# Optimization experiments

Measured on AMD Instinct MI355X. Metric: run time of the kernel, lower is better.

## Reference

```python
import jax, jax.numpy as jnp
import numpy as np

H = 128        # hidden_size == embed dim
HEADS = 8
HD = H // HEADS  # 16
OUT = 2


def _mlp(x, w1, b1, w2, b2, w3, b3):
    # build_mlps(2, [128, 64, 128], ret_before_act=True, without_norm=True)
    x = jax.nn.relu(x @ w1.T + b1)
    x = jax.nn.relu(x @ w2.T + b2)
    return x @ w3.T + b3


def _cross_attn(q, kv, mask, wq, bq, wk, bk, wv, bv, wo, bo):
    # q: [B, A, H] agent queries; kv: [B, M, H] map polylines; mask: [B, M] True = padded
    B, A, _ = q.shape
    M = kv.shape[1]
    qh = (q @ wq.T + bq).reshape(B, A, HEADS, HD)
    kh = (kv @ wk.T + bk).reshape(B, M, HEADS, HD)
    vh = (kv @ wv.T + bv).reshape(B, M, HEADS, HD)
    scores = jnp.einsum('bahd,bmhd->bham', qh, kh) * (1.0 / np.sqrt(HD))
    scores = jnp.where(mask[:, None, None, :], jnp.finfo(scores.dtype).min, scores)
    attn = jax.nn.softmax(scores, axis=-1)
    out = jnp.einsum('bham,bmhd->bahd', attn, vh).reshape(B, A, H)
    return out @ wo.T + bo


def _lstm_cell(x, h, c, avail, w_ih, w_hh, b_ih, b_hh):
    # standard torch LSTMCell math, masked update per agent availability
    gates = x @ w_ih.T + b_ih + h @ w_hh.T + b_hh
    i, f, g, o = jnp.split(gates, 4, axis=-1)
    c_new = jax.nn.sigmoid(f) * c + jax.nn.sigmoid(i) * jnp.tanh(g)
    h_new = jax.nn.sigmoid(o) * jnp.tanh(c_new)
    m = avail[..., None]
    return jnp.where(m, h_new, h), jnp.where(m, c_new, c)


def setup_inputs() -> dict:
    key = jax.random.key(0)
    B, A, M, T = 128, 64, 512, 80
    ks = jax.random.split(key, 32)
    p = lambda k, shape: (jax.random.normal(k, shape, dtype=jnp.float32) * 0.02)
    map_avails = jax.random.uniform(ks[5], (B, M)) > 0.2
    map_avails = map_avails.at[:, :8].set(True)  # guarantee non-empty attention rows
    return {
        'current_features': jax.random.normal(ks[0], (B, A, 2), dtype=jnp.float32),
        'current_availabilities': jnp.ones((B, A), dtype=bool),
        'hidden': jax.random.normal(ks[1], (B, A, H), dtype=jnp.float32),
        'context': jax.random.normal(ks[2], (B, A, H), dtype=jnp.float32),
        'map_embedding': jax.random.normal(ks[3], (B, M, H), dtype=jnp.float32),
        'map_avails': map_avails,
        'n_timesteps': T,
        # state encoder MLP: 2 -> 128 -> 64 -> 128
        'enc_w1': p(ks[6], (128, 2)),  'enc_b1': jnp.zeros((128,), jnp.float32),
        'enc_w2': p(ks[7], (64, 128)), 'enc_b2': jnp.zeros((64,), jnp.float32),
        'enc_w3': p(ks[8], (128, 64)), 'enc_b3': jnp.zeros((128,), jnp.float32),
        # cross-attention projections
        'wq': p(ks[9], (H, H)),  'bq': jnp.zeros((H,), jnp.float32),
        'wk': p(ks[10], (H, H)), 'bk': jnp.zeros((H,), jnp.float32),
        'wv': p(ks[11], (H, H)), 'bv': jnp.zeros((H,), jnp.float32),
        'wo': p(ks[12], (H, H)), 'bo': jnp.zeros((H,), jnp.float32),
        # LSTM cell (input 128, hidden 128)
        'w_ih': p(ks[13], (4 * H, H)), 'w_hh': p(ks[14], (4 * H, H)),
        'b_ih': jnp.zeros((4 * H,), jnp.float32), 'b_hh': jnp.zeros((4 * H,), jnp.float32),
        # output head
        'lin_w': p(ks[15], (OUT, H)), 'lin_b': jnp.zeros((OUT,), jnp.float32),
    }


def reference(current_features, current_availabilities, hidden, context,
              map_embedding, map_avails, n_timesteps,
              enc_w1, enc_b1, enc_w2, enc_b2, enc_w3, enc_b3,
              wq, bq, wk, bk, wv, bv, wo, bo,
              w_ih, w_hh, b_ih, b_hh, lin_w, lin_b):
    state0 = current_features[..., :2]
    cross_mask = ~map_avails

    def step(carry, _):
        state, h, c = carry
        e = _mlp(state, enc_w1, enc_b1, enc_w2, enc_b2, enc_w3, enc_b3)
        e = _cross_attn(e, map_embedding, cross_mask, wq, bq, wk, bk, wv, bv, wo, bo)
        h, c = _lstm_cell(e, h, c, current_availabilities, w_ih, w_hh, b_ih, b_hh)
        state = state + h @ lin_w.T + lin_b
        return (state, h, c), state

    _, ys = jax.lax.scan(step, (state0, hidden, context), None, length=n_timesteps)
    return jnp.moveaxis(ys, 0, 2)  # [B, A, T, 2]
```

## Files before the change

kernel.cpp:

```cpp
#include <hip/hip_runtime.h>
#include <cstdint>
#include <cstddef>


typedef short short8 __attribute__((ext_vector_type(8)));
typedef float f32x4 __attribute__((ext_vector_type(4)));

#define LOG2E 1.4426950408889634f
#define QSCALE 0.36067376022224085f

__device__ __forceinline__ unsigned short f2bf(float f) {
  union { float f; unsigned int u; } v; v.f = f;
  unsigned int u = v.u;
  return (unsigned short)((u + 0x7fffu + ((u >> 16) & 1u)) >> 16);
}
__device__ __forceinline__ float fexp2(float x) {
  return __builtin_amdgcn_exp2f(x);
}
__device__ __forceinline__ float frcp(float x) {
  return __builtin_amdgcn_rcpf(x);
}
__device__ __forceinline__ float sigm(float x) {
  return frcp(1.f + fexp2(-LOG2E * x));
}
__device__ __forceinline__ float tanh_f(float x) {
  return 1.f - 2.f * frcp(1.f + fexp2(2.f * LOG2E * x));
}
__device__ __forceinline__ f32x4 splat4(float v) { f32x4 r = {v, v, v, v}; return r; }
__device__ __forceinline__ unsigned char f2fp8(float x) {
  return (unsigned char)__builtin_amdgcn_cvt_pk_fp8_f32(x, x, 0, false);
}
__device__ __forceinline__ f32x4 mfma_fp8(long a, long b, f32x4 c) {
  return __builtin_amdgcn_mfma_f32_16x16x32_fp8_fp8(a, b, c, 0, 0, 0);
}
__device__ __forceinline__ f32x4 mfma_bf16(short8 a, short8 b, f32x4 c) {
  return __builtin_amdgcn_mfma_f32_16x16x32_bf16(a, b, c, 0, 0, 0);
}

__global__ __launch_bounds__(256) void convert_kernel(
    const float* __restrict__ w2, const float* __restrict__ whh,
    unsigned short* __restrict__ W2, unsigned short* __restrict__ WHH) {
  int i = blockIdx.x * 256 + threadIdx.x;
  if (i >= 73728) return;
  if (i < 8192) W2[i] = f2bf(w2[i]);
  else          WHH[i - 8192] = f2bf(whh[i - 8192]);
}

__global__ __launch_bounds__(256) void fold_wiho_kernel(
    const float* __restrict__ wih, const float* __restrict__ wo,
    unsigned short* __restrict__ WIHO) {
  int i = blockIdx.x * 256 + threadIdx.x;
  int r = i >> 7, d = i & 127;
  float acc = 0.f;
  for (int n = 0; n < 128; ++n) acc = fmaf(wih[r * 128 + n], wo[n * 128 + d], acc);
  WIHO[i] = f2bf(acc);
}

__global__ __launch_bounds__(256) void fold_wq3b_kernel(
    const float* __restrict__ wq, const float* __restrict__ w3,
    const float* __restrict__ b3, const float* __restrict__ bq,
    const float* __restrict__ wih, const float* __restrict__ bo,
    const float* __restrict__ bih, const float* __restrict__ bhh,
    unsigned short* __restrict__ WQ3, float* __restrict__ B4p,
    float* __restrict__ BQ3S) {
  int i = blockIdx.x * 256 + threadIdx.x;
  if (i < 8192) {
    int n = i >> 6, k = i & 63;
    float acc = 0.f;
    for (int j = 0; j < 128; ++j) acc = fmaf(wq[n * 128 + j], w3[j * 64 + k], acc);
    WQ3[i] = f2bf(acc * QSCALE);
  } else if (i < 8704) {
    int r = i - 8192;
    float acc = bih[r] + bhh[r];
    for (int n = 0; n < 128; ++n) acc = fmaf(wih[r * 128 + n], bo[n], acc);
    B4p[r] = acc;
  } else if (i < 8832) {
    int n = i - 8704;
    float acc = bq[n];
    for (int j = 0; j < 128; ++j) acc = fmaf(wq[n * 128 + j], b3[j], acc);
    BQ3S[n] = acc * QSCALE;
  }
}

__global__ __launch_bounds__(256) void kv_kernel(
    const float* __restrict__ emb, const float* __restrict__ wk,
    const float* __restrict__ bk, const float* __restrict__ wv,
    const float* __restrict__ bv,
    unsigned char* __restrict__ K8, unsigned char* __restrict__ V8) {
  extern __shared__ char smem[];
  float* s_e = (float*)smem;
  float* s_w = (float*)(smem + 33024);
  const int tid = threadIdx.x;
  const int b = blockIdx.x >> 3;
  const int m0 = (blockIdx.x & 7) * 64;

  for (int i = tid; i < 8192; i += 256) {
    int row = i >> 7, col = i & 127;
    s_e[row * 129 + col] = emb[(size_t)(b * 512 + m0 + row) * 128 + col];
  }
  for (int i = tid; i < 16384; i += 256) {
    int row = i >> 7, col = i & 127;
    s_w[row * 129 + col] = wk[i];
  }
  __syncthreads();
  {
    const int dg = tid & 31, rg = tid >> 5;
    float acc[8][4];
#pragma unroll
    for (int rr = 0; rr < 8; ++rr)
#pragma unroll
      for (int j = 0; j < 4; ++j) acc[rr][j] = 0.f;
    for (int k = 0; k < 128; ++k) {
      float e[8];
#pragma unroll
      for (int rr = 0; rr < 8; ++rr) e[rr] = s_e[(rg * 8 + rr) * 129 + k];
#pragma unroll
      for (int j = 0; j < 4; ++j) {
        float w = s_w[(dg * 4 + j) * 129 + k];
#pragma unroll
        for (int rr = 0; rr < 8; ++rr) acc[rr][j] = fmaf(e[rr], w, acc[rr][j]);
      }
    }
#pragma unroll
    for (int rr = 0; rr < 8; ++rr)
#pragma unroll
      for (int j = 0; j < 4; ++j) {
        int d = dg * 4 + j;
        K8[(size_t)(b * 512 + m0 + rg * 8 + rr) * 128 + d] = f2fp8(acc[rr][j] + bk[d]);
      }
  }
  __syncthreads();
  for (int i = tid; i < 16384; i += 256) {
    int row = i >> 7, col = i & 127;
    s_w[row * 129 + col] = wv[i];
  }
  __syncthreads();
  {
    const int r = tid & 63, dg = tid >> 6;
    float acc[32];
#pragma unroll
    for (int j = 0; j < 32; ++j) acc[j] = 0.f;
    for (int k = 0; k < 128; ++k) {
      float e = s_e[r * 129 + k];
#pragma unroll
      for (int j = 0; j < 32; ++j) acc[j] = fmaf(e, s_w[(dg * 32 + j) * 129 + k], acc[j]);
    }
    const int m = m0 + r;
    const int ml = m & 31;
    const int sperm = (ml < 16) ? (((ml >> 2) << 3) | (ml & 3))
                                : ((((ml - 16) >> 2) << 3) | ((ml - 16) & 3) | 4);
    const int mpos = (m & ~31) | sperm;
#pragma unroll
    for (int j = 0; j < 32; ++j) {
      int d = dg * 32 + j;
      V8[(size_t)(b * 128 + d) * 512 + mpos] = f2fp8(acc[j] + bv[d]);
    }
  }
}

__global__ __launch_bounds__(512, 2) void decoder_kernel(
    const float* __restrict__ cf, const int* __restrict__ cav,
    const float* __restrict__ hid,
    const float* __restrict__ ctx, const int* __restrict__ mav,
    const int* __restrict__ ntp,
    const float* __restrict__ w1, const float* __restrict__ b1,
    const float* __restrict__ b2,
    const unsigned char* __restrict__ K8, const unsigned char* __restrict__ V8,
    const unsigned short* __restrict__ W2, const unsigned short* __restrict__ WQ3,
    const unsigned short* __restrict__ WIHO, const unsigned short* __restrict__ WHH,
    const float* __restrict__ B4p, const float* __restrict__ BQ3S,
    const float* __restrict__ lnw, const float* __restrict__ lnb,
    float* __restrict__ out) {
  extern __shared__ char smem[];
  unsigned short* s_bufA = (unsigned short*)(smem + 131072);
  unsigned short* s_bufB = (unsigned short*)(smem + 139776);
  unsigned short* s_h = (unsigned short*)(smem + 148480);
  unsigned short* s_h2 = (unsigned short*)(smem + 157184);
  unsigned char* s_maskb = (unsigned char*)(smem + 162048);

  const int tid = threadIdx.x;
  const int wave = tid >> 6;
  const int lane = tid & 63;
  const int quad = lane >> 4;
  const int l16 = lane & 15;

  const int b = blockIdx.x & 127;
  const int a0 = (blockIdx.x >> 7) * 32;
  const int T = *ntp;
  const f32x4 zero4 = {0.f, 0.f, 0.f, 0.f};
  const long kOnes = 0x3838383838383838L;

  {
    const unsigned long long* Kg = (const unsigned long long*)(K8 + (size_t)b * 65536);
    for (int i = tid; i < 8192; i += 512) {
      int tok = i >> 4, seg = i & 15;
      *(unsigned long long*)(smem + tok * 128 + ((seg * 8) ^ ((tok & 15) * 8))) =
          Kg[(size_t)tok * 16 + seg];
    }
    const unsigned long long* Vg = (const unsigned long long*)(V8 + (size_t)b * 65536);
    for (int i = tid; i < 8192; i += 512) {
      int d = i >> 6, seg = i & 63;
      *(unsigned long long*)(smem + 65536 + d * 512 + ((seg * 8) ^ ((d & 15) * 8))) =
          Vg[(size_t)d * 64 + seg];
    }
  }
  s_maskb[tid] = mav[b * 512 + tid] ? 1 : 0;
  {
    int idx = tid * 8;
    int a = idx >> 7, n0 = idx & 127;
    const float* hp = hid + (size_t)(b * 64 + a0 + a) * 128 + n0;
    short8 v;
#pragma unroll
    for (int j = 0; j < 8; ++j) v[j] = (short)f2bf(hp[j]);
    *(short8*)(s_h + a * 136 + n0) = v;
  }
  float c_reg[2][4], avl[2][4];
#pragma unroll
  for (int mt = 0; mt < 2; ++mt)
#pragma unroll
    for (int r = 0; r < 4; ++r) {
      int a = mt * 16 + quad * 4 + r;
      c_reg[mt][r] = ctx[(size_t)(b * 64 + a0 + a) * 128 + wave * 16 + l16];
      avl[mt][r] = (cav[b * 64 + a0 + a] != 0) ? 1.f : 0.f;
    }

  const int wrow = wave * 16 + l16;
  short8 rIH[4][4], rHH[4][4];
#pragma unroll
  for (int kt = 0; kt < 4; ++kt)
#pragma unroll
    for (int g = 0; g < 4; ++g) {
      rIH[kt][g] = *(const short8*)(WIHO + ((g * 128 + wrow) * 128 + kt * 32 + quad * 8));
      rHH[kt][g] = *(const short8*)(WHH + ((g * 128 + wrow) * 128 + kt * 32 + quad * 8));
    }
  short8 rWQ3[2];
#pragma unroll
  for (int kt = 0; kt < 2; ++kt)
    rWQ3[kt] = *(const short8*)(WQ3 + (wrow * 64 + kt * 32 + quad * 8));
  float rB4[4];
#pragma unroll
  for (int g = 0; g < 4; ++g) rB4[g] = B4p[g * 128 + wrow];
  const float rBQ3 = BQ3S[wrow];
  const float rB2 = b2[(wave & 3) * 16 + l16];

  const int p7_o = tid >> 3, p7_sub = tid & 7;
  const int p7_a = p7_o >> 1, p7_oi = p7_o & 1;
  const float mylnb = lnb[p7_oi];
  float myst = cf[(size_t)(b * 64 + a0 + p7_a) * 2 + p7_oi];

  __syncthreads();

  unsigned mflags = 0;
#pragma unroll
  for (int i = 0; i < 32; ++i)
    if (!s_maskb[i * 16 + l16]) mflags |= (1u << i);

  {
    float other = __shfl_xor(myst, 8);
    float st0 = p7_oi ? other : myst;
    float st1 = p7_oi ? myst : other;
    int a = tid >> 4, n0 = (tid & 15) * 8;
    const float* wp = w1 + n0 * 2;
    const float* bp = b1 + n0;
    short8 v;
#pragma unroll
    for (int j = 0; j < 8; ++j) {
      float x = fmaf(wp[j * 2], st0, fmaf(wp[j * 2 + 1], st1, bp[j]));
      v[j] = (short)f2bf(fmaxf(x, 0.f));
    }
    *(short8*)(s_bufA + a * 136 + n0) = v;
  }
  __syncthreads();

#pragma unroll 1
  for (int t = 0; t < T; ++t) {
    {
      int mt = wave >> 2, nt = wave & 3;
      f32x4 acc = splat4(rB2);
#pragma unroll
      for (int kt = 0; kt < 4; ++kt) {
        short8 a8 = *(const short8*)(s_bufA + (mt * 16 + l16) * 136 + kt * 32 + quad * 8);
        short8 b8 = *(const short8*)(W2 + ((nt * 16 + l16) * 128 + kt * 32 + quad * 8));
        acc = mfma_bf16(a8, b8, acc);
      }
#pragma unroll
      for (int r = 0; r < 4; ++r)
        s_h2[(mt * 16 + quad * 4 + r) * 72 + nt * 16 + l16] = f2bf(fmaxf(acc[r], 0.f));
    }
    __syncthreads();

    unsigned char* s_q8 = (unsigned char*)s_bufA;
    {
#pragma unroll
      for (int mt = 0; mt < 2; ++mt) {
        f32x4 acc = splat4(rBQ3);
#pragma unroll
        for (int kt = 0; kt < 2; ++kt) {
          short8 a8 = *(const short8*)(s_h2 + (mt * 16 + l16) * 72 + kt * 32 + quad * 8);
          acc = mfma_bf16(a8, rWQ3[kt], acc);
        }
#pragma unroll
        for (int r = 0; r < 4; ++r)
          s_q8[(mt * 16 + quad * 4 + r) * 136 + wave * 16 + l16] = f2fp8(acc[r]);
      }
    }
    __asm__ volatile("s_waitcnt lgkmcnt(0)" ::: "memory");
    __builtin_amdgcn_sched_barrier(0);

    {
      const int h = wave;
      const char* sKb = (const char*)smem;
      const char* sVrow = (const char*)(smem + 65536) + (h * 16 + l16) * 512;
      long qA[2];
#pragma unroll
      for (int mt = 0; mt < 2; ++mt)
        qA[mt] = (quad < 2)
                     ? *(const long*)(s_q8 + (mt * 16 + l16) * 136 + h * 16 + quad * 8)
                     : (quad == 2 ? 0xF8L : 0L);
      const int koff = (h * 16 + quad * 8) ^ (l16 * 8);
      f32x4 O[2], L4[2];
      O[0] = zero4; O[1] = zero4; L4[0] = zero4; L4[1] = zero4;
      long vA_c = *(const long*)(sVrow + ((quad * 8) ^ (l16 * 8)));
      long kB_c0 = 0L, kB_c1 = 0L;
      if (quad < 2) {
        kB_c0 = *(const long*)(sKb + (size_t)l16 * 128 + koff);
        kB_c1 = *(const long*)(sKb + (size_t)(16 + l16) * 128 + koff);
      }
#pragma unroll 4
      for (int c = 0; c < 16; ++c) {
        long vA_n = 0L, kB_n0 = 0L, kB_n1 = 0L;
        if (c < 15) {
          vA_n = *(const long*)(sVrow + (((c + 1) * 32 + quad * 8) ^ (l16 * 8)));
          if (quad < 2) {
            kB_n0 = *(const long*)(sKb + (size_t)((c + 1) * 32 + l16) * 128 + koff);
            kB_n1 = *(const long*)(sKb + (size_t)((c + 1) * 32 + 16 + l16) * 128 + koff);
          }
        }
        long kB0 = kB_c0, kB1 = kB_c1;
        if (quad == 2) {
          kB0 = ((mflags >> (c * 2)) & 1u) ? 0x38L : 0L;
          kB1 = ((mflags >> (c * 2 + 1)) & 1u) ? 0x38L : 0L;
        }
        f32x4 S2[2][2];
        S2[0][0] = mfma_fp8(kB0, qA[0], zero4);
        S2[0][1] = mfma_fp8(kB0, qA[1], zero4);
        S2[1][0] = mfma_fp8(kB1, qA[0], zero4);
        S2[1][1] = mfma_fp8(kB1, qA[1], zero4);
#pragma unroll
        for (int mt = 0; mt < 2; ++mt) {
          unsigned w0 = (unsigned)__builtin_amdgcn_cvt_pk_fp8_f32(
              fexp2(S2[0][mt][0]), fexp2(S2[0][mt][1]), 0, false);
          w0 = (unsigned)__builtin_amdgcn_cvt_pk_fp8_f32(
              fexp2(S2[0][mt][2]), fexp2(S2[0][mt][3]), (int)w0, true);
          unsigned w1v = (unsigned)__builtin_amdgcn_cvt_pk_fp8_f32(
              fexp2(S2[1][mt][0]), fexp2(S2[1][mt][1]), 0, false);
          w1v = (unsigned)__builtin_amdgcn_cvt_pk_fp8_f32(
              fexp2(S2[1][mt][2]), fexp2(S2[1][mt][3]), (int)w1v, true);
          long pB = (long)(((unsigned long long)w1v << 32) | (unsigned long long)w0);
          O[mt] = mfma_fp8(vA_c, pB, O[mt]);
          L4[mt] = mfma_fp8(kOnes, pB, L4[mt]);
        }
        vA_c = vA_n; kB_c0 = kB_n0; kB_c1 = kB_n1;
      }
#pragma unroll
      for (int mt = 0; mt < 2; ++mt) {
        unsigned long long ow = 0;
#pragma unroll
        for (int r = 0; r < 4; ++r) {
          float o_r = O[mt][r] * frcp(L4[mt][r]);
          ow |= (unsigned long long)f2bf(o_r) << (16 * r);
        }
        *(unsigned long long*)(s_bufB + (mt * 16 + l16) * 136 + h * 16 + quad * 4) = ow;
      }
    }
    __syncthreads();

    {
      const int ni = wave;
      f32x4 gi[2], gf[2], gg[2], go[2];
#pragma unroll
      for (int mt = 0; mt < 2; ++mt) {
        gi[mt] = splat4(rB4[0]);
        gf[mt] = splat4(rB4[1]);
        gg[mt] = splat4(rB4[2]);
        go[mt] = splat4(rB4[3]);
      }
#pragma unroll
      for (int kt = 0; kt < 4; ++kt)
#pragma unroll
        for (int mt = 0; mt < 2; ++mt) {
          short8 a8 = *(const short8*)(s_bufB + (mt * 16 + l16) * 136 + kt * 32 + quad * 8);
          gi[mt] = mfma_bf16(a8, rIH[kt][0], gi[mt]);
          gf[mt] = mfma_bf16(a8, rIH[kt][1], gf[mt]);
          gg[mt] = mfma_bf16(a8, rIH[kt][2], gg[mt]);
          go[mt] = mfma_bf16(a8, rIH[kt][3], go[mt]);
        }
#pragma unroll
      for (int kt = 0; kt < 4; ++kt)
#pragma unroll
        for (int mt = 0; mt < 2; ++mt) {
          short8 a8 = *(const short8*)(s_h + (mt * 16 + l16) * 136 + kt * 32 + quad * 8);
          gi[mt] = mfma_bf16(a8, rHH[kt][0], gi[mt]);
          gf[mt] = mfma_bf16(a8, rHH[kt][1], gf[mt]);
          gg[mt] = mfma_bf16(a8, rHH[kt][2], gg[mt]);
          go[mt] = mfma_bf16(a8, rHH[kt][3], go[mt]);
        }
      float hnew[2][4];
#pragma unroll
      for (int mt = 0; mt < 2; ++mt)
#pragma unroll
        for (int r = 0; r < 4; ++r) {
          float iv = sigm(gi[mt][r]);
          float fv = sigm(gf[mt][r]);
          float gv = tanh_f(gg[mt][r]);
          float ov = sigm(go[mt][r]);
          float cn = fmaf(fv, c_reg[mt][r], iv * gv);
          float hv = ov * tanh_f(cn);
          int arow = mt * 16 + quad * 4 + r;
          float av = avl[mt][r];
          union { unsigned int u; float f; } ho;
          ho.u = ((unsigned int)s_h[arow * 136 + ni * 16 + l16]) << 16;
          c_reg[mt][r] = av * cn + (1.f - av) * c_reg[mt][r];
          hnew[mt][r] = av * hv + (1.f - av) * ho.f;
        }
      __syncthreads();
#pragma unroll
      for (int mt = 0; mt < 2; ++mt)
#pragma unroll
        for (int r = 0; r < 4; ++r) {
          int arow = mt * 16 + quad * 4 + r;
          s_h[arow * 136 + ni * 16 + l16] = f2bf(hnew[mt][r]);
        }
    }
    __syncthreads();

    {
      const unsigned short* hp = s_h + p7_a * 136 + p7_sub * 16;
      const float* lw = lnw + p7_oi * 128 + p7_sub * 16;
      short8 h0 = *(const short8*)hp;
      short8 h1 = *(const short8*)(hp + 8);
      float acc = 0.f;
#pragma unroll
      for (int k = 0; k < 8; ++k) {
        union { unsigned int u; float f; } hv;
        hv.u = ((unsigned int)(unsigned short)h0[k]) << 16;
        acc = fmaf(hv.f, lw[k], acc);
      }
#pragma unroll
      for (int k = 0; k < 8; ++k) {
        union { unsigned int u; float f; } hv;
        hv.u = ((unsigned int)(unsigned short)h1[k]) << 16;
        acc = fmaf(hv.f, lw[8 + k], acc);
      }
      acc += __shfl_xor(acc, 4);
      acc += __shfl_xor(acc, 2);
      acc += __shfl_xor(acc, 1);
      float ns = myst + acc + mylnb;
      myst = ns;
      if (p7_sub == 0)
        out[((size_t)(b * 64 + a0 + p7_a) * T + t) * 2 + p7_oi] = ns;
      float other = __shfl_xor(ns, 8);
      float st0 = p7_oi ? other : ns;
      float st1 = p7_oi ? ns : other;
      int a = tid >> 4, n0 = (tid & 15) * 8;
      const float* wp = w1 + n0 * 2;
      const float* bp = b1 + n0;
      short8 v;
#pragma unroll
      for (int j = 0; j < 8; ++j) {
        float x = fmaf(wp[j * 2], st0, fmaf(wp[j * 2 + 1], st1, bp[j]));
        v[j] = (short)f2bf(fmaxf(x, 0.f));
      }
      *(short8*)(s_bufA + a * 136 + n0) = v;
    }
    __syncthreads();
  }
}

extern "C" void kernel_launch(void* const* d_in, const int* in_sizes, int n_in,
                              void* d_out, int out_size, void* d_ws, size_t ws_size,
                              hipStream_t stream) {
  (void)in_sizes; (void)n_in; (void)out_size; (void)ws_size;
  const float* cf = (const float*)d_in[0];
  const int* cav = (const int*)d_in[1];
  const float* hid = (const float*)d_in[2];
  const float* ctx = (const float*)d_in[3];
  const float* emb = (const float*)d_in[4];
  const int* mav = (const int*)d_in[5];
  const int* ntp = (const int*)d_in[6];
  const float* w1 = (const float*)d_in[7];
  const float* b1 = (const float*)d_in[8];
  const float* w2 = (const float*)d_in[9];
  const float* b2 = (const float*)d_in[10];
  const float* w3 = (const float*)d_in[11];
  const float* b3 = (const float*)d_in[12];
  const float* wq = (const float*)d_in[13];
  const float* bq = (const float*)d_in[14];
  const float* wk = (const float*)d_in[15];
  const float* bk = (const float*)d_in[16];
  const float* wv = (const float*)d_in[17];
  const float* bv = (const float*)d_in[18];
  const float* wo = (const float*)d_in[19];
  const float* bo = (const float*)d_in[20];
  const float* wih = (const float*)d_in[21];
  const float* whh = (const float*)d_in[22];
  const float* bih = (const float*)d_in[23];
  const float* bhh = (const float*)d_in[24];
  const float* lnw = (const float*)d_in[25];
  const float* lnb = (const float*)d_in[26];

  char* ws = (char*)d_ws;
  unsigned char* K8 = (unsigned char*)(ws + 0);
  unsigned char* V8 = (unsigned char*)(ws + 8388608);
  unsigned short* W2s = (unsigned short*)(ws + 16777216);
  unsigned short* WQ3s = (unsigned short*)(ws + 16793600);
  unsigned short* WIHOs = (unsigned short*)(ws + 16809984);
  unsigned short* WHHs = (unsigned short*)(ws + 16941056);
  float* B4p = (float*)(ws + 17072128);
  float* BQ3S = (float*)(ws + 17074176);

  (void)hipFuncSetAttribute((const void*)kv_kernel,
                            hipFuncAttributeMaxDynamicSharedMemorySize, 99072);
  (void)hipFuncSetAttribute((const void*)decoder_kernel,
                            hipFuncAttributeMaxDynamicSharedMemorySize, 162560);

  convert_kernel<<<288, 256, 0, stream>>>(w2, whh, W2s, WHHs);
  fold_wiho_kernel<<<256, 256, 0, stream>>>(wih, wo, WIHOs);
  fold_wq3b_kernel<<<35, 256, 0, stream>>>(wq, w3, b3, bq, wih, bo, bih, bhh,
                                           WQ3s, B4p, BQ3S);
  kv_kernel<<<1024, 256, 99072, stream>>>(emb, wk, bk, wv, bv, K8, V8);
  decoder_kernel<<<256, 512, 162560, stream>>>(
      cf, cav, hid, ctx, mav, ntp, w1, b1, b2, K8, V8, W2s, WQ3s, WIHOs, WHHs,
      B4p, BQ3S, lnw, lnb, (float*)d_out);
}
```

Baseline: 1.293 ms.

## Merge prep kernels into one launch and software-pipeline the decoder step

Combines the four preprocessing kernels into one prep_kernel launch, dispatched by block index, to cut launch overhead. In the decoder's attention loop, score MFMAs are issued one chunk ahead and K loads two chunks ahead, to hide latency. Hidden-state fragments are loaded into registers at the start of each step, which lets the LSTM write the new h directly and drops one __syncthreads. The extra live registers may hurt occupancy, and prep blocks now all reserve the large shared-memory allocation.

```diff
diff --git a/kernel.cpp b/kernel.cpp
--- a/kernel.cpp
+++ b/kernel.cpp
@@ -37,123 +37,122 @@
   return __builtin_amdgcn_mfma_f32_16x16x32_bf16(a, b, c, 0, 0, 0);
 }
 
-__global__ __launch_bounds__(256) void convert_kernel(
-    const float* __restrict__ w2, const float* __restrict__ whh,
-    unsigned short* __restrict__ W2, unsigned short* __restrict__ WHH) {
-  int i = blockIdx.x * 256 + threadIdx.x;
-  if (i >= 73728) return;
-  if (i < 8192) W2[i] = f2bf(w2[i]);
-  else          WHH[i - 8192] = f2bf(whh[i - 8192]);
-}
-
-__global__ __launch_bounds__(256) void fold_wiho_kernel(
-    const float* __restrict__ wih, const float* __restrict__ wo,
-    unsigned short* __restrict__ WIHO) {
-  int i = blockIdx.x * 256 + threadIdx.x;
-  int r = i >> 7, d = i & 127;
-  float acc = 0.f;
-  for (int n = 0; n < 128; ++n) acc = fmaf(wih[r * 128 + n], wo[n * 128 + d], acc);
-  WIHO[i] = f2bf(acc);
-}
-
-__global__ __launch_bounds__(256) void fold_wq3b_kernel(
-    const float* __restrict__ wq, const float* __restrict__ w3,
-    const float* __restrict__ b3, const float* __restrict__ bq,
-    const float* __restrict__ wih, const float* __restrict__ bo,
-    const float* __restrict__ bih, const float* __restrict__ bhh,
-    unsigned short* __restrict__ WQ3, float* __restrict__ B4p,
-    float* __restrict__ BQ3S) {
-  int i = blockIdx.x * 256 + threadIdx.x;
-  if (i < 8192) {
-    int n = i >> 6, k = i & 63;
-    float acc = 0.f;
-    for (int j = 0; j < 128; ++j) acc = fmaf(wq[n * 128 + j], w3[j * 64 + k], acc);
-    WQ3[i] = f2bf(acc * QSCALE);
-  } else if (i < 8704) {
-    int r = i - 8192;
-    float acc = bih[r] + bhh[r];
-    for (int n = 0; n < 128; ++n) acc = fmaf(wih[r * 128 + n], bo[n], acc);
-    B4p[r] = acc;
-  } else if (i < 8832) {
-    int n = i - 8704;
-    float acc = bq[n];
-    for (int j = 0; j < 128; ++j) acc = fmaf(wq[n * 128 + j], b3[j], acc);
-    BQ3S[n] = acc * QSCALE;
-  }
-}
-
-__global__ __launch_bounds__(256) void kv_kernel(
+__global__ __launch_bounds__(256) void prep_kernel(
     const float* __restrict__ emb, const float* __restrict__ wk,
     const float* __restrict__ bk, const float* __restrict__ wv,
     const float* __restrict__ bv,
-    unsigned char* __restrict__ K8, unsigned char* __restrict__ V8) {
+    const float* __restrict__ w2, const float* __restrict__ whh,
+    const float* __restrict__ wih, const float* __restrict__ wo,
+    const float* __restrict__ wq, const float* __restrict__ w3,
+    const float* __restrict__ b3, const float* __restrict__ bq,
+    const float* __restrict__ bo, const float* __restrict__ bih,
+    const float* __restrict__ bhh,
+    unsigned char* __restrict__ K8, unsigned char* __restrict__ V8,
+    unsigned short* __restrict__ W2, unsigned short* __restrict__ WHH,
+    unsigned short* __restrict__ WIHO, unsigned short* __restrict__ WQ3,
+    float* __restrict__ B4p, float* __restrict__ BQ3S) {
   extern __shared__ char smem[];
-  float* s_e = (float*)smem;
-  float* s_w = (float*)(smem + 33024);
   const int tid = threadIdx.x;
-  const int b = blockIdx.x >> 3;
-  const int m0 = (blockIdx.x & 7) * 64;
-
-  for (int i = tid; i < 8192; i += 256) {
-    int row = i >> 7, col = i & 127;
-    s_e[row * 129 + col] = emb[(size_t)(b * 512 + m0 + row) * 128 + col];
-  }
-  for (int i = tid; i < 16384; i += 256) {
-    int row = i >> 7, col = i & 127;
-    s_w[row * 129 + col] = wk[i];
-  }
-  __syncthreads();
-  {
-    const int dg = tid & 31, rg = tid >> 5;
-    float acc[8][4];
-#pragma unroll
-    for (int rr = 0; rr < 8; ++rr)
-#pragma unroll
-      for (int j = 0; j < 4; ++j) acc[rr][j] = 0.f;
-    for (int k = 0; k < 128; ++k) {
-      float e[8];
-#pragma unroll
-      for (int rr = 0; rr < 8; ++rr) e[rr] = s_e[(rg * 8 + rr) * 129 + k];
-#pragma unroll
-      for (int j = 0; j < 4; ++j) {
-        float w = s_w[(dg * 4 + j) * 129 + k];
-#pragma unroll
-        for (int rr = 0; rr < 8; ++rr) acc[rr][j] = fmaf(e[rr], w, acc[rr][j]);
-      }
-    }
-#pragma unroll
-    for (int rr = 0; rr < 8; ++rr)
-#pragma unroll
-      for (int j = 0; j < 4; ++j) {
-        int d = dg * 4 + j;
-        K8[(size_t)(b * 512 + m0 + rg * 8 + rr) * 128 + d] = f2fp8(acc[rr][j] + bk[d]);
-      }
-  }
-  __syncthreads();
-  for (int i = tid; i < 16384; i += 256) {
-    int row = i >> 7, col = i & 127;
-    s_w[row * 129 + col] = wv[i];
-  }
-  __syncthreads();
-  {
-    const int r = tid & 63, dg = tid >> 6;
-    float acc[32];
-#pragma unroll
-    for (int j = 0; j < 32; ++j) acc[j] = 0.f;
-    for (int k = 0; k < 128; ++k) {
-      float e = s_e[r * 129 + k];
-#pragma unroll
-      for (int j = 0; j < 32; ++j) acc[j] = fmaf(e, s_w[(dg * 32 + j) * 129 + k], acc[j]);
-    }
-    const int m = m0 + r;
-    const int ml = m & 31;
-    const int sperm = (ml < 16) ? (((ml >> 2) << 3) | (ml & 3))
-                                : ((((ml - 16) >> 2) << 3) | ((ml - 16) & 3) | 4);
-    const int mpos = (m & ~31) | sperm;
-#pragma unroll
-    for (int j = 0; j < 32; ++j) {
-      int d = dg * 32 + j;
-      V8[(size_t)(b * 128 + d) * 512 + mpos] = f2fp8(acc[j] + bv[d]);
+  const int blk = blockIdx.x;
+
+  if (blk < 1024) {
+    float* s_e = (float*)smem;
+    float* s_w = (float*)(smem + 33024);
+    const int b = blk >> 3;
+    const int m0 = (blk & 7) * 64;
+
+    for (int i = tid; i < 8192; i += 256) {
+      int row = i >> 7, col = i & 127;
+      s_e[row * 129 + col] = emb[(size_t)(b * 512 + m0 + row) * 128 + col];
+    }
+    for (int i = tid; i < 16384; i += 256) {
+      int row = i >> 7, col = i & 127;
+      s_w[row * 129 + col] = wk[i];
+    }
+    __syncthreads();
+    {
+      const int dg = tid & 31, rg = tid >> 5;
+      float acc[8][4];
+#pragma unroll
+      for (int rr = 0; rr < 8; ++rr)
+#pragma unroll
+        for (int j = 0; j < 4; ++j) acc[rr][j] = 0.f;
+      for (int k = 0; k < 128; ++k) {
+        float e[8];
+#pragma unroll
+        for (int rr = 0; rr < 8; ++rr) e[rr] = s_e[(rg * 8 + rr) * 129 + k];
+#pragma unroll
+        for (int j = 0; j < 4; ++j) {
+          float w = s_w[(dg * 4 + j) * 129 + k];
+#pragma unroll
+          for (int rr = 0; rr < 8; ++rr) acc[rr][j] = fmaf(e[rr], w, acc[rr][j]);
+        }
+      }
+#pragma unroll
+      for (int rr = 0; rr < 8; ++rr)
+#pragma unroll
+        for (int j = 0; j < 4; ++j) {
+          int d = dg * 4 + j;
+          K8[(size_t)(b * 512 + m0 + rg * 8 + rr) * 128 + d] =
+              f2fp8(acc[rr][j] + bk[d]);
+        }
+    }
+    __syncthreads();
+    for (int i = tid; i < 16384; i += 256) {
+      int row = i >> 7, col = i & 127;
+      s_w[row * 129 + col] = wv[i];
+    }
+    __syncthreads();
+    {
+      const int r = tid & 63, dg = tid >> 6;
+      float acc[32];
+#pragma unroll
+      for (int j = 0; j < 32; ++j) acc[j] = 0.f;
+      for (int k = 0; k < 128; ++k) {
+        float e = s_e[r * 129 + k];
+#pragma unroll
+        for (int j = 0; j < 32; ++j)
+          acc[j] = fmaf(e, s_w[(dg * 32 + j) * 129 + k], acc[j]);
+      }
+      const int m = m0 + r;
+      const int ml = m & 31;
+      const int sperm = (ml < 16) ? (((ml >> 2) << 3) | (ml & 3))
+                                  : ((((ml - 16) >> 2) << 3) | ((ml - 16) & 3) | 4);
+      const int mpos = (m & ~31) | sperm;
+#pragma unroll
+      for (int j = 0; j < 32; ++j) {
+        int d = dg * 32 + j;
+        V8[(size_t)(b * 128 + d) * 512 + mpos] = f2fp8(acc[j] + bv[d]);
+      }
+    }
+  } else if (blk < 1280) {
+    int i = (blk - 1024) * 256 + tid;
+    int r = i >> 7, d = i & 127;
+    float acc = 0.f;
+    for (int n = 0; n < 128; ++n)
+      acc = fmaf(wih[r * 128 + n], wo[n * 128 + d], acc);
+    WIHO[i] = f2bf(acc);
+  } else if (blk < 1568) {
+    int i = (blk - 1280) * 256 + tid;
+    if (i < 8192) W2[i] = f2bf(w2[i]);
+    else if (i < 73728) WHH[i - 8192] = f2bf(whh[i - 8192]);
+  } else {
+    int i = (blk - 1568) * 256 + tid;
+    if (i < 8192) {
+      int n = i >> 6, k = i & 63;
+      float acc = 0.f;
+      for (int j = 0; j < 128; ++j) acc = fmaf(wq[n * 128 + j], w3[j * 64 + k], acc);
+      WQ3[i] = f2bf(acc * QSCALE);
+    } else if (i < 8704) {
+      int r = i - 8192;
+      float acc = bih[r] + bhh[r];
+      for (int n = 0; n < 128; ++n) acc = fmaf(wih[r * 128 + n], bo[n], acc);
+      B4p[r] = acc;
+    } else if (i < 8832) {
+      int n = i - 8704;
+      float acc = bq[n];
+      for (int j = 0; j < 128; ++j) acc = fmaf(wq[n * 128 + j], b3[j], acc);
+      BQ3S[n] = acc * QSCALE;
     }
   }
 }
@@ -274,6 +273,22 @@
 
 #pragma unroll 1
   for (int t = 0; t < T; ++t) {
+    short8 rHa[4][2];
+    float hoF[2][4];
+#pragma unroll
+    for (int kt = 0; kt < 4; ++kt)
+#pragma unroll
+      for (int mt = 0; mt < 2; ++mt)
+        rHa[kt][mt] = *(const short8*)(s_h + (mt * 16 + l16) * 136 + kt * 32 + quad * 8);
+#pragma unroll
+    for (int mt = 0; mt < 2; ++mt)
+#pragma unroll
+      for (int r = 0; r < 4; ++r) {
+        union { unsigned int u; float f; } ho;
+        ho.u = ((unsigned int)s_h[(mt * 16 + quad * 4 + r) * 136 + wave * 16 + l16]) << 16;
+        hoF[mt][r] = ho.f;
+      }
+
     {
       int mt = wave >> 2, nt = wave & 3;
       f32x4 acc = splat4(rB2);
@@ -318,49 +333,56 @@
                      ? *(const long*)(s_q8 + (mt * 16 + l16) * 136 + h * 16 + quad * 8)
                      : (quad == 2 ? 0xF8L : 0L);
       const int koff = (h * 16 + quad * 8) ^ (l16 * 8);
+      auto ldK = [&](int c, long& k0, long& k1) {
+        if (quad < 2) {
+          k0 = *(const long*)(sKb + (size_t)(c * 32 + l16) * 128 + koff);
+          k1 = *(const long*)(sKb + (size_t)(c * 32 + 16 + l16) * 128 + koff);
+        } else if (quad == 2) {
+          k0 = ((mflags >> (c * 2)) & 1u) ? 0x38L : 0L;
+          k1 = ((mflags >> (c * 2 + 1)) & 1u) ? 0x38L : 0L;
+        } else { k0 = 0L; k1 = 0L; }
+      };
       f32x4 O[2], L4[2];
       O[0] = zero4; O[1] = zero4; L4[0] = zero4; L4[1] = zero4;
-      long vA_c = *(const long*)(sVrow + ((quad * 8) ^ (l16 * 8)));
-      long kB_c0 = 0L, kB_c1 = 0L;
-      if (quad < 2) {
-        kB_c0 = *(const long*)(sKb + (size_t)l16 * 128 + koff);
-        kB_c1 = *(const long*)(sKb + (size_t)(16 + l16) * 128 + koff);
-      }
-#pragma unroll 4
+      long kS0, kS1, kP0, kP1;
+      ldK(0, kS0, kS1);
+      ldK(1, kP0, kP1);
+      long vAc = *(const long*)(sVrow + ((quad * 8) ^ (l16 * 8)));
+      f32x4 Sc[2][2];
+      Sc[0][0] = mfma_fp8(kS0, qA[0], zero4);
+      Sc[0][1] = mfma_fp8(kS0, qA[1], zero4);
+      Sc[1][0] = mfma_fp8(kS1, qA[0], zero4);
+      Sc[1][1] = mfma_fp8(kS1, qA[1], zero4);
+#pragma unroll 2
       for (int c = 0; c < 16; ++c) {
-        long vA_n = 0L, kB_n0 = 0L, kB_n1 = 0L;
+        long kN0 = 0L, kN1 = 0L, vAn = 0L;
+        if (c < 14) ldK(c + 2, kN0, kN1);
+        if (c < 15)
+          vAn = *(const long*)(sVrow + (((c + 1) * 32 + quad * 8) ^ (l16 * 8)));
+        f32x4 Sn[2][2];
         if (c < 15) {
-          vA_n = *(const long*)(sVrow + (((c + 1) * 32 + quad * 8) ^ (l16 * 8)));
-          if (quad < 2) {
-            kB_n0 = *(const long*)(sKb + (size_t)((c + 1) * 32 + l16) * 128 + koff);
-            kB_n1 = *(const long*)(sKb + (size_t)((c + 1) * 32 + 16 + l16) * 128 + koff);
-          }
-        }
-        long kB0 = kB_c0, kB1 = kB_c1;
-        if (quad == 2) {
-          kB0 = ((mflags >> (c * 2)) & 1u) ? 0x38L : 0L;
-          kB1 = ((mflags >> (c * 2 + 1)) & 1u) ? 0x38L : 0L;
-        }
-        f32x4 S2[2][2];
-        S2[0][0] = mfma_fp8(kB0, qA[0], zero4);
-        S2[0][1] = mfma_fp8(kB0, qA[1], zero4);
-        S2[1][0] = mfma_fp8(kB1, qA[0], zero4);
-        S2[1][1] = mfma_fp8(kB1, qA[1], zero4);
+          Sn[0][0] = mfma_fp8(kP0, qA[0], zero4);
+          Sn[0][1] = mfma_fp8(kP0, qA[1], zero4);
+          Sn[1][0] = mfma_fp8(kP1, qA[0], zero4);
+          Sn[1][1] = mfma_fp8(kP1, qA[1], zero4);
+        }
 #pragma unroll
         for (int mt = 0; mt < 2; ++mt) {
           unsigned w0 = (unsigned)__builtin_amdgcn_cvt_pk_fp8_f32(
-              fexp2(S2[0][mt][0]), fexp2(S2[0][mt][1]), 0, false);
+              fexp2(Sc[0][mt][0]), fexp2(Sc[0][mt][1]), 0, false);
           w0 = (unsigned)__builtin_amdgcn_cvt_pk_fp8_f32(
-              fexp2(S2[0][mt][2]), fexp2(S2[0][mt][3]), (int)w0, true);
+              fexp2(Sc[0][mt][2]), fexp2(Sc[0][mt][3]), (int)w0, true);
           unsigned w1v = (unsigned)__builtin_amdgcn_cvt_pk_fp8_f32(
-              fexp2(S2[1][mt][0]), fexp2(S2[1][mt][1]), 0, false);
+              fexp2(Sc[1][mt][0]), fexp2(Sc[1][mt][1]), 0, false);
           w1v = (unsigned)__builtin_amdgcn_cvt_pk_fp8_f32(
-              fexp2(S2[1][mt][2]), fexp2(S2[1][mt][3]), (int)w1v, true);
+              fexp2(Sc[1][mt][2]), fexp2(Sc[1][mt][3]), (int)w1v, true);
           long pB = (long)(((unsigned long long)w1v << 32) | (unsigned long long)w0);
-          O[mt] = mfma_fp8(vA_c, pB, O[mt]);
+          O[mt] = mfma_fp8(vAc, pB, O[mt]);
           L4[mt] = mfma_fp8(kOnes, pB, L4[mt]);
         }
-        vA_c = vA_n; kB_c0 = kB_n0; kB_c1 = kB_n1;
+        Sc[0][0] = Sn[0][0]; Sc[0][1] = Sn[0][1];
+        Sc[1][0] = Sn[1][0]; Sc[1][1] = Sn[1][1];
+        kP0 = kN0; kP1 = kN1; vAc = vAn;
       }
 #pragma unroll
       for (int mt = 0; mt < 2; ++mt) {
@@ -377,6 +399,12 @@
 
     {
       const int ni = wave;
+      short8 oa8[4][2];
+#pragma unroll
+      for (int kt = 0; kt < 4; ++kt)
+#pragma unroll
+        for (int mt = 0; mt < 2; ++mt)
+          oa8[kt][mt] = *(const short8*)(s_bufB + (mt * 16 + l16) * 136 + kt * 32 + quad * 8);
       f32x4 gi[2], gf[2], gg[2], go[2];
 #pragma unroll
       for (int mt = 0; mt < 2; ++mt) {
@@ -389,23 +417,20 @@
       for (int kt = 0; kt < 4; ++kt)
 #pragma unroll
         for (int mt = 0; mt < 2; ++mt) {
-          short8 a8 = *(const short8*)(s_bufB + (mt * 16 + l16) * 136 + kt * 32 + quad * 8);
-          gi[mt] = mfma_bf16(a8, rIH[kt][0], gi[mt]);
-          gf[mt] = mfma_bf16(a8, rIH[kt][1], gf[mt]);
-          gg[mt] = mfma_bf16(a8, rIH[kt][2], gg[mt]);
-          go[mt] = mfma_bf16(a8, rIH[kt][3], go[mt]);
+          gi[mt] = mfma_bf16(oa8[kt][mt], rIH[kt][0], gi[mt]);
+          gf[mt] = mfma_bf16(oa8[kt][mt], rIH[kt][1], gf[mt]);
+          gg[mt] = mfma_bf16(oa8[kt][mt], rIH[kt][2], gg[mt]);
+          go[mt] = mfma_bf16(oa8[kt][mt], rIH[kt][3], go[mt]);
         }
 #pragma unroll
       for (int kt = 0; kt < 4; ++kt)
 #pragma unroll
         for (int mt = 0; mt < 2; ++mt) {
-          short8 a8 = *(const short8*)(s_h + (mt * 16 + l16) * 136 + kt * 32 + quad * 8);
-          gi[mt] = mfma_bf16(a8, rHH[kt][0], gi[mt]);
-          gf[mt] = mfma_bf16(a8, rHH[kt][1], gf[mt]);
-          gg[mt] = mfma_bf16(a8, rHH[kt][2], gg[mt]);
-          go[mt] = mfma_bf16(a8, rHH[kt][3], go[mt]);
-        }
-      float hnew[2][4];
+          gi[mt] = mfma_bf16(rHa[kt][mt], rHH[kt][0], gi[mt]);
+          gf[mt] = mfma_bf16(rHa[kt][mt], rHH[kt][1], gf[mt]);
+          gg[mt] = mfma_bf16(rHa[kt][mt], rHH[kt][2], gg[mt]);
+          go[mt] = mfma_bf16(rHa[kt][mt], rHH[kt][3], go[mt]);
+        }
 #pragma unroll
       for (int mt = 0; mt < 2; ++mt)
 #pragma unroll
@@ -416,20 +441,11 @@
           float ov = sigm(go[mt][r]);
           float cn = fmaf(fv, c_reg[mt][r], iv * gv);
           float hv = ov * tanh_f(cn);
+          float av = avl[mt][r];
+          c_reg[mt][r] = av * cn + (1.f - av) * c_reg[mt][r];
+          float hn = av * hv + (1.f - av) * hoF[mt][r];
           int arow = mt * 16 + quad * 4 + r;
-          float av = avl[mt][r];
-          union { unsigned int u; float f; } ho;
-          ho.u = ((unsigned int)s_h[arow * 136 + ni * 16 + l16]) << 16;
-          c_reg[mt][r] = av * cn + (1.f - av) * c_reg[mt][r];
-          hnew[mt][r] = av * hv + (1.f - av) * ho.f;
-        }
-      __syncthreads();
-#pragma unroll
-      for (int mt = 0; mt < 2; ++mt)
-#pragma unroll
-        for (int r = 0; r < 4; ++r) {
-          int arow = mt * 16 + quad * 4 + r;
-          s_h[arow * 136 + ni * 16 + l16] = f2bf(hnew[mt][r]);
+          s_h[arow * 136 + ni * 16 + l16] = f2bf(hn);
         }
     }
     __syncthreads();
@@ -519,16 +535,14 @@
   float* B4p = (float*)(ws + 17072128);
   float* BQ3S = (float*)(ws + 17074176);
 
-  (void)hipFuncSetAttribute((const void*)kv_kernel,
+  (void)hipFuncSetAttribute((const void*)prep_kernel,
                             hipFuncAttributeMaxDynamicSharedMemorySize, 99072);
   (void)hipFuncSetAttribute((const void*)decoder_kernel,
                             hipFuncAttributeMaxDynamicSharedMemorySize, 162560);
 
-  convert_kernel<<<288, 256, 0, stream>>>(w2, whh, W2s, WHHs);
-  fold_wiho_kernel<<<256, 256, 0, stream>>>(wih, wo, WIHOs);
-  fold_wq3b_kernel<<<35, 256, 0, stream>>>(wq, w3, b3, bq, wih, bo, bih, bhh,
-                                           WQ3s, B4p, BQ3S);
-  kv_kernel<<<1024, 256, 99072, stream>>>(emb, wk, bk, wv, bv, K8, V8);
+  prep_kernel<<<1603, 256, 99072, stream>>>(
+      emb, wk, bk, wv, bv, w2, whh, wih, wo, wq, w3, b3, bq, bo, bih, bhh,
+      K8, V8, W2s, WHHs, WIHOs, WQ3s, B4p, BQ3S);
   decoder_kernel<<<256, 512, 162560, stream>>>(
       cf, cav, hid, ctx, mav, ntp, w1, b1, b2, K8, V8, W2s, WQ3s, WIHOs, WHHs,
       B4p, BQ3S, lnw, lnb, (float*)d_out);
```

After: 2.125 ms. 64.3% more time.
